# Performance work log

Measured on AMD Instinct MI355X. Metric: run time of the kernel, lower is better.

The kernel has to match this reference:

```python
import jax, jax.numpy as jnp
import numpy as np
import math

EMBED_DIM = 1024
NUM_HEADS = 16
HEAD_DIM = EMBED_DIM // NUM_HEADS


def setup_inputs() -> dict:
    key = jax.random.key(0)
    ks = jax.random.split(key, 9)
    B, S, D = 4, 2048, EMBED_DIM
    s = 1.0 / math.sqrt(D)
    x = jax.random.normal(ks[0], (B, S, D), dtype=jnp.float32)
    Wq = jax.random.normal(ks[1], (D, D), dtype=jnp.float32) * s
    bq = jnp.zeros((D,), dtype=jnp.float32)
    Wk = jax.random.normal(ks[2], (D, D), dtype=jnp.float32) * s
    bk = jnp.zeros((D,), dtype=jnp.float32)
    Wv = jax.random.normal(ks[3], (D, D), dtype=jnp.float32) * s
    bv = jnp.zeros((D,), dtype=jnp.float32)
    Wo = jax.random.normal(ks[4], (D, D), dtype=jnp.float32) * s
    bo = jnp.zeros((D,), dtype=jnp.float32)
    return {"x": x, "Wq": Wq, "bq": bq, "Wk": Wk, "bk": bk,
            "Wv": Wv, "bv": bv, "Wo": Wo, "bo": bo}


def reference(x, Wq, bq, Wk, bk, Wv, bv, Wo, bo):
    B, S, D = x.shape
    H, hd = NUM_HEADS, HEAD_DIM
    # projections: [B,S,D] -> [B,H,S,hd]
    def split_heads(t):
        return t.reshape(B, S, H, hd).transpose(0, 2, 1, 3)
    Q = split_heads(x @ Wq + bq)
    K = split_heads(x @ Wk + bk)
    V = split_heads(x @ Wv + bv)
    scale = 1.0 / math.sqrt(hd)
    scores = jnp.einsum('bhqd,bhkd->bhqk', Q, K) * scale  # [B,H,S,S]
    causal = jnp.tril(jnp.ones((S, S), dtype=bool))
    scores = jnp.where(causal, scores, -jnp.inf)
    attn = jax.nn.softmax(scores, axis=-1)
    out = jnp.einsum('bhqk,bhkd->bhqd', attn, V)  # [B,H,S,hd]
    out = out.transpose(0, 2, 1, 3).reshape(B, S, D)
    return out @ Wo + bo
```

## Files before the change

kernel.cpp:

```cpp
#include <hip/hip_runtime.h>
#include <hip/hip_bf16.h>
#include <cstdint>
#include <cstddef>

typedef __bf16 bf16_t;
typedef __bf16 bf16x4 __attribute__((ext_vector_type(4)));
typedef __bf16 bf16x8 __attribute__((ext_vector_type(8)));
typedef float f32x4 __attribute__((ext_vector_type(4)));
typedef float f32x16 __attribute__((ext_vector_type(16)));
typedef unsigned u32x2 __attribute__((ext_vector_type(2)));

typedef __attribute__((address_space(1))) void as1_void_t;
typedef __attribute__((address_space(3))) void as3_void_t;

__device__ __forceinline__ void gload_lds16(const bf16_t* g, bf16_t* l) {
  __builtin_amdgcn_global_load_lds((as1_void_t*)g, (as3_void_t*)l, 16, 0, 0);
}

__global__ __launch_bounds__(256) void prep_k(
    const float* __restrict__ x,
    const float* __restrict__ wq, const float* __restrict__ wk,
    const float* __restrict__ wv, const float* __restrict__ wo,
    bf16_t* __restrict__ xb, bf16_t* __restrict__ wqt,
    bf16_t* __restrict__ wkt, bf16_t* __restrict__ wvt, bf16_t* __restrict__ wot)
{
  __shared__ float t[64][65];
  if (blockIdx.x < 2048) {
    const int tid = blockIdx.x * 256 + threadIdx.x;
    const int NX4 = (8192 * 1024) / 4;
    for (int i = tid; i < NX4; i += 2048 * 256) {
      float4 v = ((const float4*)x)[i];
      bf16x4 o;
      o[0] = (bf16_t)v.x; o[1] = (bf16_t)v.y; o[2] = (bf16_t)v.z; o[3] = (bf16_t)v.w;
      ((bf16x4*)xb)[i] = o;
    }
  } else {
    const int tile = blockIdx.x - 2048;
    const int tr = tile >> 4, tc = tile & 15;
    const int c = threadIdx.x & 63, r4 = threadIdx.x >> 6;
#pragma unroll 1
    for (int zz = 0; zz < 4; ++zz) {
      const float* w = (zz == 0) ? wq : (zz == 1) ? wk : (zz == 2) ? wv : wo;
      bf16_t* wt = (zz == 0) ? wqt : (zz == 1) ? wkt : (zz == 2) ? wvt : wot;
#pragma unroll
      for (int rr = 0; rr < 16; ++rr) {
        int row = rr * 4 + r4;
        t[row][c] = w[(size_t)(tr * 64 + row) * 1024 + tc * 64 + c];
      }
      __syncthreads();
#pragma unroll
      for (int rr = 0; rr < 16; ++rr) {
        int row = rr * 4 + r4;
        wt[(size_t)(tc * 64 + row) * 1024 + tr * 64 + c] = (bf16_t)t[c][row];
      }
      __syncthreads();
    }
  }
}

constexpr int BM = 128, BN = 128, BK = 64;

template <int MODE>
__global__ __launch_bounds__(256) void gemm_proj_k(
    const bf16_t* __restrict__ A,
    const bf16_t* __restrict__ W0T, const bf16_t* __restrict__ W1T,
    const float* __restrict__ b0, const float* __restrict__ b1,
    bf16_t* __restrict__ o0, bf16_t* __restrict__ o1)
{
  constexpr int K = 1024;
  __shared__ bf16_t a_lds[BM * BK];
  __shared__ bf16_t b_lds[BN * BK];
  const int z = blockIdx.z;
  const bf16_t* Bt = (z == 0) ? W0T : W1T;
  const float* bias = (z == 0) ? b0 : b1;
  bf16_t* outp = (z == 0) ? o0 : o1;
  const float oscale = (MODE == 0 && z == 0) ? 0.18033688011112042f : 1.0f;

  const int tid = threadIdx.x;
  const int l = tid & 63;
  const int wv = tid >> 6;
  const int wr = wv >> 1, wc = wv & 1;
  const int lr = l & 15, lg = l >> 4;
  const int bm = blockIdx.x * BM;
  const int bn = blockIdx.y * BN;

  f32x4 acc[4][4] = {};

  const int srow = tid >> 3;
  const int scc = tid & 7;

  for (int k0 = 0; k0 < K; k0 += BK) {
    __syncthreads();
#pragma unroll
    for (int it = 0; it < 4; ++it) {
      int row = srow + it * 32;
      int gk = (scc ^ (row & 7)) * 8;
      gload_lds16(A + (size_t)(bm + row) * K + k0 + gk, a_lds + row * BK + scc * 8);
      gload_lds16(Bt + (size_t)(bn + row) * K + k0 + gk, b_lds + row * BK + scc * 8);
    }
    __syncthreads();
#pragma unroll
    for (int kk = 0; kk < 2; ++kk) {
      bf16x8 af[4], bfr[4];
#pragma unroll
      for (int m = 0; m < 4; ++m) {
        int row = wr * 64 + m * 16 + lr;
        int ch = (kk * 4 + lg) ^ (row & 7);
        af[m] = *(const bf16x8*)&a_lds[row * BK + ch * 8];
      }
#pragma unroll
      for (int n = 0; n < 4; ++n) {
        int row = wc * 64 + n * 16 + lr;
        int ch = (kk * 4 + lg) ^ (row & 7);
        bfr[n] = *(const bf16x8*)&b_lds[row * BK + ch * 8];
      }
#pragma unroll
      for (int m = 0; m < 4; ++m)
#pragma unroll
        for (int n = 0; n < 4; ++n) {
          if constexpr (MODE == 0)
            acc[m][n] = __builtin_amdgcn_mfma_f32_16x16x32_bf16(bfr[n], af[m], acc[m][n], 0, 0, 0);
          else
            acc[m][n] = __builtin_amdgcn_mfma_f32_16x16x32_bf16(af[m], bfr[n], acc[m][n], 0, 0, 0);
        }
    }
  }

  if constexpr (MODE == 0) {
#pragma unroll
    for (int m = 0; m < 4; ++m) {
      const int row = bm + wr * 64 + m * 16 + lr;
      const int bhb = row >> 11, seq = row & 2047;
#pragma unroll
      for (int n = 0; n < 4; ++n) {
        const int col0 = bn + wc * 64 + n * 16 + lg * 4;
        const float4 b4 = *(const float4*)&bias[col0];
        const int bh = bhb * 16 + (col0 >> 6);
        const int dl0 = col0 & 63;
        size_t off = (((size_t)(bh * 64 + (seq >> 5)) * 4 + (dl0 >> 4)) * 64
                      + (((dl0 >> 3) & 1) * 32 + (seq & 31))) * 8 + (dl0 & 7);
        bf16x4 o4;
        o4[0] = (bf16_t)((acc[m][n][0] + b4.x) * oscale);
        o4[1] = (bf16_t)((acc[m][n][1] + b4.y) * oscale);
        o4[2] = (bf16_t)((acc[m][n][2] + b4.z) * oscale);
        o4[3] = (bf16_t)((acc[m][n][3] + b4.w) * oscale);
        *(bf16x4*)&outp[off] = o4;
      }
    }
  } else {
#pragma unroll
    for (int n = 0; n < 4; ++n) {
      const int col = bn + wc * 64 + n * 16 + lr;
      const float bv_ = bias[col];
      const int dl = col & 63;
#pragma unroll
      for (int m = 0; m < 4; ++m) {
        const int row0 = bm + wr * 64 + m * 16 + lg * 4;
        const int bhb = row0 >> 11, seq0 = row0 & 2047;
        const int bh = bhb * 16 + (col >> 6);
        size_t off = ((((size_t)(bh * 64 + (seq0 >> 5)) * 2 + (dl >> 5)) * 2
                       + ((seq0 >> 4) & 1)) * 64
                      + (((seq0 >> 3) & 1) * 32 + (dl & 31))) * 8 + (seq0 & 7);
        bf16x4 o4;
        o4[0] = (bf16_t)(acc[m][n][0] + bv_);
        o4[1] = (bf16_t)(acc[m][n][1] + bv_);
        o4[2] = (bf16_t)(acc[m][n][2] + bv_);
        o4[3] = (bf16_t)(acc[m][n][3] + bv_);
        *(bf16x4*)&outp[off] = o4;
      }
    }
  }
}

__global__ __launch_bounds__(256) void gemm_o_k(
    const bf16_t* __restrict__ A, const bf16_t* __restrict__ Bt,
    const float* __restrict__ bias, float* __restrict__ outp)
{
  constexpr int K = 1024;
  __shared__ bf16_t a_lds[BM * BK];
  __shared__ bf16_t b_lds[BN * BK];
  const int tid = threadIdx.x;
  const int l = tid & 63;
  const int wv = tid >> 6;
  const int wr = wv >> 1, wc = wv & 1;
  const int lr = l & 15, lg = l >> 4;
  const int bm = blockIdx.x * BM;
  const int bn = blockIdx.y * BN;

  f32x4 acc[4][4] = {};
  const int srow = tid >> 3;
  const int scc = tid & 7;

  for (int k0 = 0; k0 < K; k0 += BK) {
    __syncthreads();
#pragma unroll
    for (int it = 0; it < 4; ++it) {
      int row = srow + it * 32;
      int gk = (scc ^ (row & 7)) * 8;
      gload_lds16(A + (size_t)(bm + row) * K + k0 + gk, a_lds + row * BK + scc * 8);
      gload_lds16(Bt + (size_t)(bn + row) * K + k0 + gk, b_lds + row * BK + scc * 8);
    }
    __syncthreads();
#pragma unroll
    for (int kk = 0; kk < 2; ++kk) {
      bf16x8 af[4], bfr[4];
#pragma unroll
      for (int m = 0; m < 4; ++m) {
        int row = wr * 64 + m * 16 + lr;
        int ch = (kk * 4 + lg) ^ (row & 7);
        af[m] = *(const bf16x8*)&a_lds[row * BK + ch * 8];
      }
#pragma unroll
      for (int n = 0; n < 4; ++n) {
        int row = wc * 64 + n * 16 + lr;
        int ch = (kk * 4 + lg) ^ (row & 7);
        bfr[n] = *(const bf16x8*)&b_lds[row * BK + ch * 8];
      }
#pragma unroll
      for (int m = 0; m < 4; ++m)
#pragma unroll
        for (int n = 0; n < 4; ++n)
          acc[m][n] = __builtin_amdgcn_mfma_f32_16x16x32_bf16(bfr[n], af[m], acc[m][n], 0, 0, 0);
    }
  }

#pragma unroll
  for (int m = 0; m < 4; ++m) {
    const int row = bm + wr * 64 + m * 16 + lr;
#pragma unroll
    for (int n = 0; n < 4; ++n) {
      const int col0 = bn + wc * 64 + n * 16 + lg * 4;
      const float4 b4 = *(const float4*)&bias[col0];
      float4 o4;
      o4.x = acc[m][n][0] + b4.x;
      o4.y = acc[m][n][1] + b4.y;
      o4.z = acc[m][n][2] + b4.z;
      o4.w = acc[m][n][3] + b4.w;
      *(float4*)&outp[(size_t)row * 1024 + col0] = o4;
    }
  }
}

__device__ __forceinline__ unsigned pack2bf(float a, float b) {
  union { bf16_t h[2]; unsigned u; } z;
  z.h[0] = (bf16_t)a; z.h[1] = (bf16_t)b;
  return z.u;
}

__device__ __forceinline__ void permswap(unsigned& a, unsigned& b) {
  u32x2 r = __builtin_amdgcn_permlane32_swap(a, b, false, false);
  a = r[0]; b = r[1];
}

__device__ __forceinline__ float xadd32(float x) {
  unsigned a = __float_as_uint(x), b = __float_as_uint(x);
  permswap(a, b);
  return __uint_as_float(a) + __uint_as_float(b);
}

__device__ __forceinline__ void sm_pv(
    const f32x16& st, const bf16x8 vf[2][2], f32x16 oacc[2], float& ls)
{
  float p[16];
#pragma unroll
  for (int r = 0; r < 16; ++r) p[r] = __builtin_amdgcn_exp2f(st[r]);
  float s0 = (p[0] + p[1]) + (p[2] + p[3]);
  float s1 = (p[4] + p[5]) + (p[6] + p[7]);
  float s2 = (p[8] + p[9]) + (p[10] + p[11]);
  float s3 = (p[12] + p[13]) + (p[14] + p[15]);
  ls += ((s0 + s1) + (s2 + s3));

  bf16x8 pf[2];
#pragma unroll
  for (int ks = 0; ks < 2; ++ks) {
    unsigned a0 = pack2bf(p[8 * ks + 0], p[8 * ks + 1]);
    unsigned a1 = pack2bf(p[8 * ks + 2], p[8 * ks + 3]);
    unsigned b0 = pack2bf(p[8 * ks + 4], p[8 * ks + 5]);
    unsigned b1 = pack2bf(p[8 * ks + 6], p[8 * ks + 7]);
    permswap(a0, b0);
    permswap(a1, b1);
    union { unsigned wd[4]; bf16x8 v; } zz;
    zz.wd[0] = a0; zz.wd[1] = a1; zz.wd[2] = b0; zz.wd[3] = b1;
    pf[ks] = zz.v;
  }
  __builtin_amdgcn_s_setprio(1);
#pragma unroll
  for (int dt = 0; dt < 2; ++dt)
#pragma unroll
    for (int ks = 0; ks < 2; ++ks)
      oacc[dt] = __builtin_amdgcn_mfma_f32_32x32x16_bf16(vf[dt][ks], pf[ks], oacc[dt], 0, 0, 0);
  __builtin_amdgcn_s_setprio(0);
}

__global__ __launch_bounds__(256) void attn_k(
    const bf16_t* __restrict__ Q, const bf16_t* __restrict__ Kmat,
    const bf16_t* __restrict__ Vt, bf16_t* __restrict__ O)
{
  const int bh = blockIdx.x;
  const int by = blockIdx.y;
  const int tid = threadIdx.x;
  const int l = tid & 63;
  const int w = tid >> 6;
  const int idx = by * 4 + w;
  const int t1 = idx, t2 = 63 - idx;
  const int t2max = 63 - by * 4;
  const int NP = (t2max + 1) >> 1;
  const int qb1 = t1 * 32, qb2 = t2 * 32;
  const int lc = l & 31;
  const int hi = l >> 5;

  __shared__ bf16_t kbuf[3][4096];
  __shared__ bf16_t vbuf[3][4096];

  const bf16_t* Kg = Kmat + (size_t)bh * 131072;
  const bf16_t* Vg = Vt + (size_t)bh * 131072;
  const bf16_t* Qf = Q + (size_t)bh * 131072 + l * 8;

  bf16x8 qf1[4], qf2[4];
#pragma unroll
  for (int ds = 0; ds < 4; ++ds) {
    qf1[ds] = *(const bf16x8*)&Qf[(size_t)(t1 * 4 + ds) * 512];
    qf2[ds] = *(const bf16x8*)&Qf[(size_t)(t2 * 4 + ds) * 512];
  }

  float ls1 = 0.f, ls2 = 0.f;
  f32x16 o1[2] = {}, o2[2] = {};

  auto stage = [&](int p, int slot) {
    int c = (p < NP) ? p : NP - 1;
    const bf16_t* kg = Kg + (size_t)c * 4096 + tid * 8;
    const bf16_t* vg = Vg + (size_t)c * 4096 + tid * 8;
    gload_lds16(kg,        &kbuf[slot][tid * 8]);
    gload_lds16(kg + 2048, &kbuf[slot][2048 + tid * 8]);
    gload_lds16(vg,        &vbuf[slot][tid * 8]);
    gload_lds16(vg + 2048, &vbuf[slot][2048 + tid * 8]);
  };

  auto dotile = [&](const bf16_t* kb, const bf16_t* vb, int s) {
    bf16x8 kf[4];
#pragma unroll
    for (int ds = 0; ds < 4; ++ds) kf[ds] = *(const bf16x8*)&kb[ds * 512];
    bf16x8 vf[2][2];
#pragma unroll
    for (int dt = 0; dt < 2; ++dt)
#pragma unroll
      for (int ks = 0; ks < 2; ++ks)
        vf[dt][ks] = *(const bf16x8*)&vb[(dt * 2 + ks) * 512];

    f32x16 st2 = {};
    __builtin_amdgcn_s_setprio(1);
#pragma unroll
    for (int ds = 0; ds < 4; ++ds)
      st2 = __builtin_amdgcn_mfma_f32_32x32x16_bf16(kf[ds], qf2[ds], st2, 0, 0, 0);
    __builtin_amdgcn_s_setprio(0);
    const bool d1 = (s <= t1);
    f32x16 st1 = {};
    if (d1) {
      __builtin_amdgcn_s_setprio(1);
#pragma unroll
      for (int ds = 0; ds < 4; ++ds)
        st1 = __builtin_amdgcn_mfma_f32_32x32x16_bf16(kf[ds], qf1[ds], st1, 0, 0, 0);
      __builtin_amdgcn_s_setprio(0);
    }
    if (s == t2) {
#pragma unroll
      for (int r = 0; r < 16; ++r) {
        int kvloc = (r & 3) + 8 * (r >> 2) + 4 * hi;
        if (kvloc > lc) st2[r] = -1e30f;
      }
    }
    if (d1 && s == t1) {
#pragma unroll
      for (int r = 0; r < 16; ++r) {
        int kvloc = (r & 3) + 8 * (r >> 2) + 4 * hi;
        if (kvloc > lc) st1[r] = -1e30f;
      }
    }
    sm_pv(st2, vf, o2, ls2);
    if (d1) sm_pv(st1, vf, o1, ls1);
  };

  stage(0, 0);
  stage(1, 1);

  int slot_c = 0;
  int slot_n = 2;
  for (int p = 0; p < NP; ++p) {
    asm volatile("s_waitcnt vmcnt(4)" ::: "memory");
    __builtin_amdgcn_s_barrier();
    __builtin_amdgcn_sched_barrier(0);
    stage(p + 2, slot_n);

    const int s0 = 2 * p;
    const bf16_t* kb = &kbuf[slot_c][l * 8];
    const bf16_t* vb = &vbuf[slot_c][l * 8];
    if (s0 <= t2) dotile(kb, vb, s0);
    if (s0 + 1 <= t2) dotile(kb + 2048, vb + 2048, s0 + 1);

    slot_c = (slot_c == 2) ? 0 : slot_c + 1;
    slot_n = (slot_n == 2) ? 0 : slot_n + 1;
  }
  asm volatile("s_waitcnt vmcnt(0)" ::: "memory");

  const int b = bh >> 4, h = bh & 15;
  {
    const float inv = 1.0f / xadd32(ls1);
    const size_t rowoff = (size_t)(b * 2048 + qb1 + lc) * 1024 + h * 64;
#pragma unroll
    for (int dt = 0; dt < 2; ++dt)
#pragma unroll
      for (int g = 0; g < 4; ++g) {
        bf16x4 o4;
#pragma unroll
        for (int t = 0; t < 4; ++t) o4[t] = (bf16_t)(o1[dt][g * 4 + t] * inv);
        *(bf16x4*)&O[rowoff + dt * 32 + g * 8 + hi * 4] = o4;
      }
  }
  {
    const float inv = 1.0f / xadd32(ls2);
    const size_t rowoff = (size_t)(b * 2048 + qb2 + lc) * 1024 + h * 64;
#pragma unroll
    for (int dt = 0; dt < 2; ++dt)
#pragma unroll
      for (int g = 0; g < 4; ++g) {
        bf16x4 o4;
#pragma unroll
        for (int t = 0; t < 4; ++t) o4[t] = (bf16_t)(o2[dt][g * 4 + t] * inv);
        *(bf16x4*)&O[rowoff + dt * 32 + g * 8 + hi * 4] = o4;
      }
  }
}

extern "C" void kernel_launch(void* const* d_in, const int* in_sizes, int n_in,
                              void* d_out, int out_size, void* d_ws, size_t ws_size,
                              hipStream_t stream)
{
  (void)in_sizes; (void)n_in; (void)out_size; (void)ws_size;
  const float* x  = (const float*)d_in[0];
  const float* Wq = (const float*)d_in[1];
  const float* bq = (const float*)d_in[2];
  const float* Wk = (const float*)d_in[3];
  const float* bk = (const float*)d_in[4];
  const float* Wv = (const float*)d_in[5];
  const float* bv = (const float*)d_in[6];
  const float* Wo = (const float*)d_in[7];
  const float* bo = (const float*)d_in[8];

  char* ws = (char*)d_ws;
  bf16_t* xb   = (bf16_t*)(ws);
  bf16_t* wqt  = (bf16_t*)(ws + (size_t)(16u << 20));
  bf16_t* wkt  = (bf16_t*)(ws + (size_t)(18u << 20));
  bf16_t* wvt  = (bf16_t*)(ws + (size_t)(20u << 20));
  bf16_t* wot  = (bf16_t*)(ws + (size_t)(22u << 20));
  bf16_t* qws  = (bf16_t*)(ws + (size_t)(24u << 20));
  bf16_t* kws  = (bf16_t*)(ws + (size_t)(40u << 20));
  bf16_t* vtws = (bf16_t*)(ws + (size_t)(56u << 20));

  prep_k<<<2304, 256, 0, stream>>>(x, Wq, Wk, Wv, Wo, xb, wqt, wkt, wvt, wot);

  dim3 gqk(8192 / BM, 1024 / BN, 2);
  gemm_proj_k<0><<<gqk, 256, 0, stream>>>(xb, wqt, wkt, bq, bk, qws, kws);
  dim3 gv(8192 / BM, 1024 / BN, 1);
  gemm_proj_k<1><<<gv, 256, 0, stream>>>(xb, wvt, wvt, bv, bv, vtws, vtws);

  attn_k<<<dim3(64, 8), 256, 0, stream>>>(qws, kws, vtws, xb);

  dim3 go(8192 / BM, 1024 / BN);
  gemm_o_k<<<go, 256, 0, stream>>>(xb, wot, bo, (float*)d_out);
}
```

Baseline: 185.0 us.

## Replace paired causal tiles with one tile per wave, heaviest blocks first

Each wave of the attention kernel previously handled two 32-row query tiles (t and 63-t) for load balancing. Now each wave handles a single query tile, the grid doubles to 16 row-blocks per head, and blockIdx.y is reversed so the longest causal blocks launch first. The LDS ring shrinks from triple to double buffering with a full vmcnt(0) wait, and loads past NP are no longer clamped. This gives more blocks and lower register and LDS use, at the cost of halving K/V tile reuse per LDS load and exposing more load latency.

```diff
diff --git a/kernel.cpp b/kernel.cpp
--- a/kernel.cpp
+++ b/kernel.cpp
@@ -297,39 +297,34 @@
     const bf16_t* __restrict__ Vt, bf16_t* __restrict__ O)
 {
   const int bh = blockIdx.x;
-  const int by = blockIdx.y;
+  const int by = 15 - blockIdx.y;
   const int tid = threadIdx.x;
   const int l = tid & 63;
   const int w = tid >> 6;
-  const int idx = by * 4 + w;
-  const int t1 = idx, t2 = 63 - idx;
-  const int t2max = 63 - by * 4;
-  const int NP = (t2max + 1) >> 1;
-  const int qb1 = t1 * 32, qb2 = t2 * 32;
+  const int t = 4 * by + w;
+  const int NP = 2 * by + 2;
+  const int qb = t * 32;
   const int lc = l & 31;
   const int hi = l >> 5;
 
-  __shared__ bf16_t kbuf[3][4096];
-  __shared__ bf16_t vbuf[3][4096];
+  __shared__ bf16_t kbuf[2][4096];
+  __shared__ bf16_t vbuf[2][4096];
 
   const bf16_t* Kg = Kmat + (size_t)bh * 131072;
   const bf16_t* Vg = Vt + (size_t)bh * 131072;
   const bf16_t* Qf = Q + (size_t)bh * 131072 + l * 8;
 
-  bf16x8 qf1[4], qf2[4];
-#pragma unroll
-  for (int ds = 0; ds < 4; ++ds) {
-    qf1[ds] = *(const bf16x8*)&Qf[(size_t)(t1 * 4 + ds) * 512];
-    qf2[ds] = *(const bf16x8*)&Qf[(size_t)(t2 * 4 + ds) * 512];
-  }
-
-  float ls1 = 0.f, ls2 = 0.f;
-  f32x16 o1[2] = {}, o2[2] = {};
+  bf16x8 qf[4];
+#pragma unroll
+  for (int ds = 0; ds < 4; ++ds)
+    qf[ds] = *(const bf16x8*)&Qf[(size_t)(t * 4 + ds) * 512];
+
+  float ls = 0.f;
+  f32x16 oa[2] = {};
 
   auto stage = [&](int p, int slot) {
-    int c = (p < NP) ? p : NP - 1;
-    const bf16_t* kg = Kg + (size_t)c * 4096 + tid * 8;
-    const bf16_t* vg = Vg + (size_t)c * 4096 + tid * 8;
+    const bf16_t* kg = Kg + (size_t)p * 4096 + tid * 8;
+    const bf16_t* vg = Vg + (size_t)p * 4096 + tid * 8;
     gload_lds16(kg,        &kbuf[slot][tid * 8]);
     gload_lds16(kg + 2048, &kbuf[slot][2048 + tid * 8]);
     gload_lds16(vg,        &vbuf[slot][tid * 8]);
@@ -347,88 +342,49 @@
       for (int ks = 0; ks < 2; ++ks)
         vf[dt][ks] = *(const bf16x8*)&vb[(dt * 2 + ks) * 512];
 
-    f32x16 st2 = {};
+    f32x16 st = {};
     __builtin_amdgcn_s_setprio(1);
 #pragma unroll
     for (int ds = 0; ds < 4; ++ds)
-      st2 = __builtin_amdgcn_mfma_f32_32x32x16_bf16(kf[ds], qf2[ds], st2, 0, 0, 0);
+      st = __builtin_amdgcn_mfma_f32_32x32x16_bf16(kf[ds], qf[ds], st, 0, 0, 0);
     __builtin_amdgcn_s_setprio(0);
-    const bool d1 = (s <= t1);
-    f32x16 st1 = {};
-    if (d1) {
-      __builtin_amdgcn_s_setprio(1);
-#pragma unroll
-      for (int ds = 0; ds < 4; ++ds)
-        st1 = __builtin_amdgcn_mfma_f32_32x32x16_bf16(kf[ds], qf1[ds], st1, 0, 0, 0);
-      __builtin_amdgcn_s_setprio(0);
-    }
-    if (s == t2) {
+    if (s == t) {
 #pragma unroll
       for (int r = 0; r < 16; ++r) {
         int kvloc = (r & 3) + 8 * (r >> 2) + 4 * hi;
-        if (kvloc > lc) st2[r] = -1e30f;
-      }
-    }
-    if (d1 && s == t1) {
-#pragma unroll
-      for (int r = 0; r < 16; ++r) {
-        int kvloc = (r & 3) + 8 * (r >> 2) + 4 * hi;
-        if (kvloc > lc) st1[r] = -1e30f;
-      }
-    }
-    sm_pv(st2, vf, o2, ls2);
-    if (d1) sm_pv(st1, vf, o1, ls1);
+        if (kvloc > lc) st[r] = -1e30f;
+      }
+    }
+    sm_pv(st, vf, oa, ls);
   };
 
   stage(0, 0);
-  stage(1, 1);
-
-  int slot_c = 0;
-  int slot_n = 2;
+
   for (int p = 0; p < NP; ++p) {
-    asm volatile("s_waitcnt vmcnt(4)" ::: "memory");
+    asm volatile("s_waitcnt vmcnt(0)" ::: "memory");
     __builtin_amdgcn_s_barrier();
     __builtin_amdgcn_sched_barrier(0);
-    stage(p + 2, slot_n);
+    if (p + 1 < NP) stage(p + 1, (p + 1) & 1);
 
     const int s0 = 2 * p;
-    const bf16_t* kb = &kbuf[slot_c][l * 8];
-    const bf16_t* vb = &vbuf[slot_c][l * 8];
-    if (s0 <= t2) dotile(kb, vb, s0);
-    if (s0 + 1 <= t2) dotile(kb + 2048, vb + 2048, s0 + 1);
-
-    slot_c = (slot_c == 2) ? 0 : slot_c + 1;
-    slot_n = (slot_n == 2) ? 0 : slot_n + 1;
-  }
-  asm volatile("s_waitcnt vmcnt(0)" ::: "memory");
+    const bf16_t* kb = &kbuf[p & 1][l * 8];
+    const bf16_t* vb = &vbuf[p & 1][l * 8];
+    if (s0 <= t) dotile(kb, vb, s0);
+    if (s0 + 1 <= t) dotile(kb + 2048, vb + 2048, s0 + 1);
+  }
 
   const int b = bh >> 4, h = bh & 15;
-  {
-    const float inv = 1.0f / xadd32(ls1);
-    const size_t rowoff = (size_t)(b * 2048 + qb1 + lc) * 1024 + h * 64;
-#pragma unroll
-    for (int dt = 0; dt < 2; ++dt)
-#pragma unroll
-      for (int g = 0; g < 4; ++g) {
-        bf16x4 o4;
-#pragma unroll
-        for (int t = 0; t < 4; ++t) o4[t] = (bf16_t)(o1[dt][g * 4 + t] * inv);
-        *(bf16x4*)&O[rowoff + dt * 32 + g * 8 + hi * 4] = o4;
-      }
-  }
-  {
-    const float inv = 1.0f / xadd32(ls2);
-    const size_t rowoff = (size_t)(b * 2048 + qb2 + lc) * 1024 + h * 64;
-#pragma unroll
-    for (int dt = 0; dt < 2; ++dt)
-#pragma unroll
-      for (int g = 0; g < 4; ++g) {
-        bf16x4 o4;
-#pragma unroll
-        for (int t = 0; t < 4; ++t) o4[t] = (bf16_t)(o2[dt][g * 4 + t] * inv);
-        *(bf16x4*)&O[rowoff + dt * 32 + g * 8 + hi * 4] = o4;
-      }
-  }
+  const float inv = 1.0f / xadd32(ls);
+  const size_t rowoff = (size_t)(b * 2048 + qb + lc) * 1024 + h * 64;
+#pragma unroll
+  for (int dt = 0; dt < 2; ++dt)
+#pragma unroll
+    for (int g = 0; g < 4; ++g) {
+      bf16x4 o4;
+#pragma unroll
+      for (int tt = 0; tt < 4; ++tt) o4[tt] = (bf16_t)(oa[dt][g * 4 + tt] * inv);
+      *(bf16x4*)&O[rowoff + dt * 32 + g * 8 + hi * 4] = o4;
+    }
 }
 
 extern "C" void kernel_launch(void* const* d_in, const int* in_sizes, int n_in,
@@ -463,7 +419,7 @@
   dim3 gv(8192 / BM, 1024 / BN, 1);
   gemm_proj_k<1><<<gv, 256, 0, stream>>>(xb, wvt, wvt, bv, bv, vtws, vtws);
 
-  attn_k<<<dim3(64, 8), 256, 0, stream>>>(qws, kws, vtws, xb);
+  attn_k<<<dim3(64, 16), 256, 0, stream>>>(qws, kws, vtws, xb);
 
   dim3 go(8192 / BM, 1024 / BN);
   gemm_o_k<<<go, 256, 0, stream>>>(xb, wot, bo, (float*)d_out);
```

Result: faster. 176.6 us, median of 2 (-4.5%).

## Rebalance causal tile assignment across waves and switch to double-buffered KV staging

Applied to the files above, without the earlier changes.

Query tiles are reassigned so the four waves in a block cover adjacent upper tiles, giving them nearly equal causal work instead of widely differing extents. KV staging moves from a three-slot ring with a partial wait to a two-slot double buffer with a full wait, and loads beyond the block's range are no longer issued. This cuts LDS use, which may allow higher occupancy and removes intra-block imbalance, but it shortens how far global loads can run ahead of compute.

```diff
diff --git a/kernel.cpp b/kernel.cpp
--- a/kernel.cpp
+++ b/kernel.cpp
@@ -297,20 +297,19 @@
     const bf16_t* __restrict__ Vt, bf16_t* __restrict__ O)
 {
   const int bh = blockIdx.x;
-  const int by = blockIdx.y;
+  const int g = blockIdx.y;
   const int tid = threadIdx.x;
   const int l = tid & 63;
   const int w = tid >> 6;
-  const int idx = by * 4 + w;
-  const int t1 = idx, t2 = 63 - idx;
-  const int t2max = 63 - by * 4;
-  const int NP = (t2max + 1) >> 1;
+  const int t1 = 4 * g + w;
+  const int t2 = 60 - 4 * g + w;
+  const int NP = 32 - 2 * g;
   const int qb1 = t1 * 32, qb2 = t2 * 32;
   const int lc = l & 31;
   const int hi = l >> 5;
 
-  __shared__ bf16_t kbuf[3][4096];
-  __shared__ bf16_t vbuf[3][4096];
+  __shared__ bf16_t kbuf[2][4096];
+  __shared__ bf16_t vbuf[2][4096];
 
   const bf16_t* Kg = Kmat + (size_t)bh * 131072;
   const bf16_t* Vg = Vt + (size_t)bh * 131072;
@@ -327,9 +326,8 @@
   f32x16 o1[2] = {}, o2[2] = {};
 
   auto stage = [&](int p, int slot) {
-    int c = (p < NP) ? p : NP - 1;
-    const bf16_t* kg = Kg + (size_t)c * 4096 + tid * 8;
-    const bf16_t* vg = Vg + (size_t)c * 4096 + tid * 8;
+    const bf16_t* kg = Kg + (size_t)p * 4096 + tid * 8;
+    const bf16_t* vg = Vg + (size_t)p * 4096 + tid * 8;
     gload_lds16(kg,        &kbuf[slot][tid * 8]);
     gload_lds16(kg + 2048, &kbuf[slot][2048 + tid * 8]);
     gload_lds16(vg,        &vbuf[slot][tid * 8]);
@@ -337,6 +335,7 @@
   };
 
   auto dotile = [&](const bf16_t* kb, const bf16_t* vb, int s) {
+    if (s > t2) return;
     bf16x8 kf[4];
 #pragma unroll
     for (int ds = 0; ds < 4; ++ds) kf[ds] = *(const bf16x8*)&kb[ds * 512];
@@ -381,26 +380,19 @@
   };
 
   stage(0, 0);
-  stage(1, 1);
-
-  int slot_c = 0;
-  int slot_n = 2;
+
   for (int p = 0; p < NP; ++p) {
-    asm volatile("s_waitcnt vmcnt(4)" ::: "memory");
+    asm volatile("s_waitcnt vmcnt(0)" ::: "memory");
     __builtin_amdgcn_s_barrier();
     __builtin_amdgcn_sched_barrier(0);
-    stage(p + 2, slot_n);
+    if (p + 1 < NP) stage(p + 1, (p + 1) & 1);
 
     const int s0 = 2 * p;
-    const bf16_t* kb = &kbuf[slot_c][l * 8];
-    const bf16_t* vb = &vbuf[slot_c][l * 8];
-    if (s0 <= t2) dotile(kb, vb, s0);
-    if (s0 + 1 <= t2) dotile(kb + 2048, vb + 2048, s0 + 1);
-
-    slot_c = (slot_c == 2) ? 0 : slot_c + 1;
-    slot_n = (slot_n == 2) ? 0 : slot_n + 1;
-  }
-  asm volatile("s_waitcnt vmcnt(0)" ::: "memory");
+    const bf16_t* kb = &kbuf[p & 1][l * 8];
+    const bf16_t* vb = &vbuf[p & 1][l * 8];
+    dotile(kb, vb, s0);
+    dotile(kb + 2048, vb + 2048, s0 + 1);
+  }
 
   const int b = bh >> 4, h = bh & 15;
   {
@@ -409,11 +401,11 @@
 #pragma unroll
     for (int dt = 0; dt < 2; ++dt)
 #pragma unroll
-      for (int g = 0; g < 4; ++g) {
+      for (int gg = 0; gg < 4; ++gg) {
         bf16x4 o4;
 #pragma unroll
-        for (int t = 0; t < 4; ++t) o4[t] = (bf16_t)(o1[dt][g * 4 + t] * inv);
-        *(bf16x4*)&O[rowoff + dt * 32 + g * 8 + hi * 4] = o4;
+        for (int tt = 0; tt < 4; ++tt) o4[tt] = (bf16_t)(o1[dt][gg * 4 + tt] * inv);
+        *(bf16x4*)&O[rowoff + dt * 32 + gg * 8 + hi * 4] = o4;
       }
   }
   {
@@ -422,11 +414,11 @@
 #pragma unroll
     for (int dt = 0; dt < 2; ++dt)
 #pragma unroll
-      for (int g = 0; g < 4; ++g) {
+      for (int gg = 0; gg < 4; ++gg) {
         bf16x4 o4;
 #pragma unroll
-        for (int t = 0; t < 4; ++t) o4[t] = (bf16_t)(o2[dt][g * 4 + t] * inv);
-        *(bf16x4*)&O[rowoff + dt * 32 + g * 8 + hi * 4] = o4;
+        for (int tt = 0; tt < 4; ++tt) o4[tt] = (bf16_t)(o2[dt][gg * 4 + tt] * inv);
+        *(bf16x4*)&O[rowoff + dt * 32 + gg * 8 + hi * 4] = o4;
       }
   }
 }
```

Result: no change. 184.9 us (-0.0%).
